# Kernel tuning notes

Hardware: AMD Instinct MI355X
Metric: run time of the kernel (lower is better)

## Reference

```python
import jax, jax.numpy as jnp
import numpy as np

D_MODEL = 2048
D_INNER = 4096
D_STATE = 16
DT_RANK = 128
D_CONV = 4
EPS = 1e-5


def setup_inputs() -> dict:
    key = jax.random.key(0)
    ks = jax.random.split(key, 10)
    b, l = 1, 1024
    s = 0.02
    x = jax.random.normal(ks[0], (b, l, D_MODEL), jnp.float32)
    w_norm = jnp.ones((D_MODEL,), jnp.float32)
    W_in = jax.random.normal(ks[1], (D_MODEL, 2 * D_INNER), jnp.float32) * s
    conv_w = jax.random.normal(ks[2], (D_CONV, D_INNER), jnp.float32) * 0.3
    conv_b = jnp.zeros((D_INNER,), jnp.float32)
    W_xp = jax.random.normal(ks[3], (D_INNER, DT_RANK + 2 * D_STATE), jnp.float32) * s
    W_dt = jax.random.normal(ks[4], (DT_RANK, D_INNER), jnp.float32) * s
    b_dt = jnp.full((D_INNER,), -4.0, jnp.float32)  # softplus(-4) ~ small dt
    A_log = jnp.log(jnp.tile(jnp.arange(1, D_STATE + 1, dtype=jnp.float32), (D_INNER, 1)))
    D = jnp.ones((D_INNER,), jnp.float32)
    W_out = jax.random.normal(ks[5], (D_INNER, D_MODEL), jnp.float32) * s
    return dict(x=x, w_norm=w_norm, W_in=W_in, conv_w=conv_w, conv_b=conv_b,
                W_xp=W_xp, W_dt=W_dt, b_dt=b_dt, A_log=A_log, D=D, W_out=W_out)


def _rmsnorm(x, w):
    return x * jax.lax.rsqrt(jnp.mean(jnp.square(x), axis=-1, keepdims=True) + EPS) * w


def _depthwise_causal_conv(x, conv_w, conv_b):
    # x: (b, l, d_inner), conv_w: (d_conv, d_inner)
    k = conv_w[:, None, :]  # (W, I/groups=1, O)
    y = jax.lax.conv_general_dilated(
        x, k, window_strides=(1,), padding=((D_CONV - 1, 0),),
        dimension_numbers=('NWC', 'WIO', 'NWC'), feature_group_count=D_INNER)
    return y + conv_b


def _selective_scan(u, delta, A, B, C, D):
    # u, delta: (b,l,d); A: (d,n); B,C: (b,l,n); D: (d,)
    deltaA = jnp.exp(jnp.einsum('bld,dn->bldn', delta, A))          # (b,l,d,n)
    deltaBu = jnp.einsum('bld,bln,bld->bldn', delta, B, u)          # (b,l,d,n)
    dA = jnp.moveaxis(deltaA, 1, 0)    # (l,b,d,n)
    dBu = jnp.moveaxis(deltaBu, 1, 0)  # (l,b,d,n)
    Ct = jnp.moveaxis(C, 1, 0)         # (l,b,n)
    b, l, d = u.shape
    n = A.shape[1]

    def step(h, inputs):
        dA_t, dBu_t, C_t = inputs
        h = h * dA_t + dBu_t                       # (b,d,n)
        y = jnp.einsum('bdn,bn->bd', h, C_t)       # (b,d)
        return h, y

    h0 = jnp.zeros((b, d, n), u.dtype)
    _, ys = jax.lax.scan(step, h0, (dA, dBu, Ct))
    y = jnp.moveaxis(ys, 0, 1)                     # (b,l,d)
    return y + u * D


def reference(x, w_norm, W_in, conv_w, conv_b, W_xp, W_dt, b_dt, A_log, D, W_out):
    # ResidualBlock: out = MambaBlock(RMSNorm(x)) + x
    xn = _rmsnorm(x, w_norm)
    xz = xn @ W_in                                  # (b,l,2*d_inner)
    xs, res = jnp.split(xz, 2, axis=-1)
    xs = _depthwise_causal_conv(xs, conv_w, conv_b)
    xs = jax.nn.silu(xs)
    # SSM
    A = -jnp.exp(A_log)                             # (d_inner, n)
    xdbc = xs @ W_xp                                # (b,l,dt_rank+2n)
    dt_r = xdbc[..., :DT_RANK]
    B = xdbc[..., DT_RANK:DT_RANK + D_STATE]
    C = xdbc[..., DT_RANK + D_STATE:]
    delta = jax.nn.softplus(dt_r @ W_dt + b_dt)     # (b,l,d_inner)
    y = _selective_scan(xs, delta, A, B, C, D)
    y = y * jax.nn.silu(res)
    out = y @ W_out + x
    return out
```

## Files before the change

kernel.cpp:

```cpp
#include <hip/hip_runtime.h>
#include <math.h>

#define L_SEQ   1024
#define DMODEL  2048
#define DINNER  4096
#define DSTATE  16
#define DTRANK  128
#define N_XZ    (2 * DINNER)
#define N_XP    (DTRANK + 2 * DSTATE)
#define EPS_F   1e-5f
#define NCHUNK  32
#define TCH     32
#define SK_XP   16

using bf16x8 = __attribute__((ext_vector_type(8))) short;
using f32x4  = __attribute__((ext_vector_type(4))) float;

__device__ __forceinline__ float silu_f(float v) {
    return v * (1.0f / (1.0f + __expf(-v)));
}
__device__ __forceinline__ float softplus_f(float v) {
    return (v > 15.0f) ? v : log1pf(__expf(v));
}
__device__ __forceinline__ unsigned short f2bf(float f) {
    unsigned b = __float_as_uint(f);
    return (unsigned short)((b + 0x7FFFu + ((b >> 16) & 1u)) >> 16);
}
__device__ __forceinline__ float bf2f(unsigned short u) {
    return __uint_as_float((unsigned)u << 16);
}

#define GLOAD_LDS(gp, lp) \
    __builtin_amdgcn_global_load_lds((const __attribute__((address_space(1))) void*)(gp), \
                                     (__attribute__((address_space(3))) void*)(lp), 16, 0, 0)

__device__ __forceinline__ void transpose_blocked(const float* __restrict__ W,
                                                  unsigned short* __restrict__ BTb,
                                                  int K, int N, int bx, int by,
                                                  unsigned short* Tb) {
    const int tid = threadIdx.x;
    const int n0 = bx * 64, k0 = by * 128;
    #pragma unroll
    for (int i = 0; i < 8; ++i) {
        const int r = i * 16 + (tid >> 4);
        const int c = (tid & 15) * 4;
        float4 v = *(const float4*)&W[(size_t)(k0 + r) * N + n0 + c];
        Tb[(c + 0) * 136 + r] = f2bf(v.x);
        Tb[(c + 1) * 136 + r] = f2bf(v.y);
        Tb[(c + 2) * 136 + r] = f2bf(v.z);
        Tb[(c + 3) * 136 + r] = f2bf(v.w);
    }
    __syncthreads();
    const int wave = tid >> 6, lane = tid & 63;
    const int kblocks = K >> 5;
    #pragma unroll
    for (int t = 0; t < 4; ++t) {
        const int ob = wave * 4 + t;
        const int nb = ob >> 2, kb = ob & 3;
        const int n = nb * 16 + (lane >> 2);
        const int k = kb * 32 + (lane & 3) * 8;
        bf16x8 v = *(const bf16x8*)&Tb[n * 136 + k];
        const size_t blk = (size_t)(((n0 >> 4) + nb)) * kblocks + ((k0 >> 5) + kb);
        *(bf16x8*)&BTb[blk * 512 + (size_t)lane * 8] = v;
    }
}

__device__ __forceinline__ void transpose_fast(const float* __restrict__ W,
                                               unsigned short* __restrict__ BT,
                                               int K, int N, int bx, int by) {
    const int wave = threadIdx.x >> 6, lane = threadIdx.x & 63;
    const int lr = lane >> 3, lc = lane & 7;
    const int k0 = by * 128 + (wave >> 1) * 64 + lr * 8;
    const int n0 = bx * 128 + (wave & 1) * 64 + lc * 8;
    float v[8][8];
    #pragma unroll
    for (int j = 0; j < 8; ++j) {
        float4 a = *(const float4*)&W[(size_t)(k0 + j) * N + n0];
        float4 b = *(const float4*)&W[(size_t)(k0 + j) * N + n0 + 4];
        v[j][0] = a.x; v[j][1] = a.y; v[j][2] = a.z; v[j][3] = a.w;
        v[j][4] = b.x; v[j][5] = b.y; v[j][6] = b.z; v[j][7] = b.w;
    }
    #pragma unroll
    for (int i = 0; i < 8; ++i) {
        bf16x8 o;
        #pragma unroll
        for (int j = 0; j < 8; ++j) o[j] = (short)f2bf(v[j][i]);
        *(bf16x8*)&BT[(size_t)(n0 + i) * K + k0] = o;
    }
}

__device__ __forceinline__ void transpose_body(const float* __restrict__ W,
                                               unsigned short* __restrict__ BT,
                                               int K, int N, int bx, int by,
                                               unsigned short (*Tl)[72]) {
    const int k0 = by * 64, n0 = bx * 32;
    const int kr = threadIdx.x >> 3;
    const int nc = (threadIdx.x & 7) * 4;
    float4 v0 = *(const float4*)&W[(size_t)(k0 + kr) * N + n0 + nc];
    float4 v1 = *(const float4*)&W[(size_t)(k0 + kr + 32) * N + n0 + nc];
    Tl[nc + 0][kr] = f2bf(v0.x); Tl[nc + 1][kr] = f2bf(v0.y);
    Tl[nc + 2][kr] = f2bf(v0.z); Tl[nc + 3][kr] = f2bf(v0.w);
    Tl[nc + 0][kr + 32] = f2bf(v1.x); Tl[nc + 1][kr + 32] = f2bf(v1.y);
    Tl[nc + 2][kr + 32] = f2bf(v1.z); Tl[nc + 3][kr + 32] = f2bf(v1.w);
    __syncthreads();
    const int n = threadIdx.x >> 3;
    const int k8 = (threadIdx.x & 7) * 8;
    *(bf16x8*)&BT[(size_t)(n0 + n) * K + k0 + k8] = *(const bf16x8*)&Tl[n][k8];
}

__global__ __launch_bounds__(256) void prep_win_kernel(const float* __restrict__ W_in,
                                                       unsigned short* __restrict__ BT_in) {
    __shared__ __align__(16) unsigned short Tb[64 * 136];
    transpose_blocked(W_in, BT_in, DMODEL, N_XZ, blockIdx.x & 127, blockIdx.x >> 7, Tb);
}

__global__ __launch_bounds__(256) void prep_rest_kernel(const float* __restrict__ W_xp,
                                                        const float* __restrict__ W_dt,
                                                        const float* __restrict__ W_out,
                                                        const float* __restrict__ x,
                                                        const float* __restrict__ wn,
                                                        unsigned short* __restrict__ BTxp,
                                                        unsigned short* __restrict__ BTdt,
                                                        unsigned short* __restrict__ BT_out,
                                                        unsigned short* __restrict__ xn_bf) {
    __shared__ __align__(16) unsigned short Tb[64 * 136];
    __shared__ unsigned short Tl[32][72];
    __shared__ float red[4];
    int b = blockIdx.x;
    if (b < 1024) {
        transpose_blocked(W_out, BT_out, DINNER, DMODEL, b & 31, b >> 5, Tb);
    } else if (b < 1056) {
        b -= 1024;
        transpose_fast(W_dt, BTdt, DTRANK, DINNER, b, 0);
    } else if (b < 1376) {
        b -= 1056;
        transpose_body(W_xp, BTxp, DINNER, N_XP, b % 5, b / 5, Tl);
    } else {
        const int row = b - 1376;
        const float4* xr = (const float4*)(x + (size_t)row * DMODEL);
        float ss = 0.f;
        float4 v0 = xr[threadIdx.x];
        float4 v1 = xr[threadIdx.x + 256];
        ss += v0.x*v0.x + v0.y*v0.y + v0.z*v0.z + v0.w*v0.w;
        ss += v1.x*v1.x + v1.y*v1.y + v1.z*v1.z + v1.w*v1.w;
        #pragma unroll
        for (int o = 32; o > 0; o >>= 1) ss += __shfl_down(ss, o);
        const int lane = threadIdx.x & 63, wv = threadIdx.x >> 6;
        if (lane == 0) red[wv] = ss;
        __syncthreads();
        if (threadIdx.x == 0) {
            float t = red[0] + red[1] + red[2] + red[3];
            red[0] = rsqrtf(t / (float)DMODEL + EPS_F);
        }
        __syncthreads();
        const float scale = red[0];
        const float4* wr = (const float4*)wn;
        float4 w0 = wr[threadIdx.x];
        float4 w1 = wr[threadIdx.x + 256];
        ushort4 o0, o1;
        o0.x = f2bf(v0.x * scale * w0.x); o0.y = f2bf(v0.y * scale * w0.y);
        o0.z = f2bf(v0.z * scale * w0.z); o0.w = f2bf(v0.w * scale * w0.w);
        o1.x = f2bf(v1.x * scale * w1.x); o1.y = f2bf(v1.y * scale * w1.y);
        o1.z = f2bf(v1.z * scale * w1.z); o1.w = f2bf(v1.w * scale * w1.w);
        unsigned short* outr = xn_bf + (size_t)row * DMODEL;
        *(ushort4*)&outr[threadIdx.x * 4] = o0;
        *(ushort4*)&outr[1024 + threadIdx.x * 4] = o1;
    }
}

template <int BM, int BN, int KC, int OUTM, int BLK>
__global__ __launch_bounds__(256) void gemm_mfma_kernel(const unsigned short* __restrict__ A,
                                                        const unsigned short* __restrict__ BT,
                                                        void* __restrict__ Cv,
                                                        int K, int Kc, int ldc, int Ncols,
                                                        const float* __restrict__ aux) {
    constexpr int MT = BM / 32;
    constexpr int NT = BN / 32;
    __shared__ __align__(16) unsigned short Al[KC * BM * 32];
    __shared__ __align__(16) unsigned short Bl[KC * BN * 32];
    const int tid = threadIdx.x;
    const int lane = tid & 63, wave = tid >> 6;
    const int wm = wave >> 1, wn = wave & 1;
    const int bm = blockIdx.y * BM, bn = blockIdx.x * BN;
    const size_t koff = (size_t)blockIdx.z * Kc;
    float* Cf = (float*)Cv;
    if (OUTM == 2) Cf += (size_t)blockIdx.z * (size_t)gridDim.y * BM * ldc;
    const int sr = lane >> 2;
    const int sk = (((lane & 3) ^ ((sr >> 1) & 3))) * 8;
    const int fr = lane & 15;
    const int fq = lane >> 4;
    const int fsw = (fq ^ ((fr >> 1) & 3)) * 8;

    f32x4 acc[MT][NT];
    #pragma unroll
    for (int i = 0; i < MT; ++i)
        #pragma unroll
        for (int j = 0; j < NT; ++j)
            acc[i][j] = (f32x4){0.f, 0.f, 0.f, 0.f};

    for (int k0 = 0; k0 < Kc; k0 += 32 * KC) {
        #pragma unroll
        for (int p = 0; p < KC; ++p) {
            #pragma unroll
            for (int is = wave; is < BM / 16; is += 4)
                GLOAD_LDS(&A[(size_t)(bm + is * 16 + sr) * K + koff + k0 + p * 32 + sk],
                          &Al[p * BM * 32 + is * 512]);
            #pragma unroll
            for (int is = wave; is < BN / 16; is += 4) {
                if (BLK) {
                    const size_t blk = (size_t)((bn >> 4) + is) * (K >> 5)
                                     + ((koff + k0 + p * 32) >> 5);
                    GLOAD_LDS(&BT[blk * 512 + sr * 32 + sk],
                              &Bl[p * BN * 32 + is * 512]);
                } else {
                    GLOAD_LDS(&BT[(size_t)(bn + is * 16 + sr) * K + koff + k0 + p * 32 + sk],
                              &Bl[p * BN * 32 + is * 512]);
                }
            }
        }
        __syncthreads();
        #pragma unroll
        for (int p = 0; p < KC; ++p) {
            bf16x8 af[MT], bfr[NT];
            #pragma unroll
            for (int i = 0; i < MT; ++i)
                af[i] = *(const bf16x8*)&Al[p * BM * 32 + (wm * (BM / 2) + i * 16 + fr) * 32 + fsw];
            #pragma unroll
            for (int j = 0; j < NT; ++j)
                bfr[j] = *(const bf16x8*)&Bl[p * BN * 32 + (wn * (BN / 2) + j * 16 + fr) * 32 + fsw];
            #pragma unroll
            for (int i = 0; i < MT; ++i)
                #pragma unroll
                for (int j = 0; j < NT; ++j)
                    acc[i][j] = __builtin_amdgcn_mfma_f32_16x16x32_bf16(af[i], bfr[j], acc[i][j], 0, 0, 0);
        }
        __syncthreads();
    }

    #pragma unroll
    for (int i = 0; i < MT; ++i) {
        const int row = bm + wm * (BM / 2) + i * 16 + fq * 4;
        #pragma unroll
        for (int j = 0; j < NT; ++j) {
            const int col = bn + wn * (BN / 2) + j * 16 + fr;
            if (col < Ncols) {
                #pragma unroll
                for (int r = 0; r < 4; ++r) {
                    float v = acc[i][j][r];
                    if (OUTM == 0) {
                        ((unsigned short*)Cv)[(size_t)(row + r) * ldc + col] = f2bf(v);
                    } else {
                        Cf[(size_t)(row + r) * ldc + col] = v;
                    }
                }
            }
        }
    }
}

__global__ __launch_bounds__(256) void gemm_k128_softplus_kernel(
        const unsigned short* __restrict__ A,
        const unsigned short* __restrict__ BT,
        unsigned short* __restrict__ C,
        const float* __restrict__ bias) {
    const int lane = threadIdx.x & 63, wave = threadIdx.x >> 6;
    const int wm = wave >> 1, wn = wave & 1;
    const int fr = lane & 15, fq = lane >> 4;
    const int bm = blockIdx.y * 64, bn = blockIdx.x * 64;

    bf16x8 af[2][4], bfr[2][4];
    #pragma unroll
    for (int i = 0; i < 2; ++i) {
        const unsigned short* Ap = &A[(size_t)(bm + wm * 32 + i * 16 + fr) * DTRANK + fq * 8];
        #pragma unroll
        for (int kc = 0; kc < 4; ++kc) af[i][kc] = *(const bf16x8*)&Ap[kc * 32];
    }
    #pragma unroll
    for (int j = 0; j < 2; ++j) {
        const unsigned short* Bp = &BT[(size_t)(bn + wn * 32 + j * 16 + fr) * DTRANK + fq * 8];
        #pragma unroll
        for (int kc = 0; kc < 4; ++kc) bfr[j][kc] = *(const bf16x8*)&Bp[kc * 32];
    }

    f32x4 acc[2][2];
    #pragma unroll
    for (int i = 0; i < 2; ++i)
        #pragma unroll
        for (int j = 0; j < 2; ++j)
            acc[i][j] = (f32x4){0.f, 0.f, 0.f, 0.f};
    #pragma unroll
    for (int kc = 0; kc < 4; ++kc)
        #pragma unroll
        for (int i = 0; i < 2; ++i)
            #pragma unroll
            for (int j = 0; j < 2; ++j)
                acc[i][j] = __builtin_amdgcn_mfma_f32_16x16x32_bf16(af[i][kc], bfr[j][kc], acc[i][j], 0, 0, 0);

    #pragma unroll
    for (int i = 0; i < 2; ++i) {
        const int row = bm + wm * 32 + i * 16 + fq * 4;
        #pragma unroll
        for (int j = 0; j < 2; ++j) {
            const int col = bn + wn * 32 + j * 16 + fr;
            const float bc = bias[col];
            #pragma unroll
            for (int r = 0; r < 4; ++r)
                C[(size_t)(row + r) * DINNER + col] = f2bf(softplus_f(acc[i][j][r] + bc));
        }
    }
}

__global__ __launch_bounds__(256) void conv_silu_kernel(const unsigned short* __restrict__ xz_bf,
                                                        const float* __restrict__ cw,
                                                        const float* __restrict__ cb,
                                                        unsigned short* __restrict__ xs_bf) {
    const int idx = blockIdx.x * 256 + threadIdx.x;
    const int t = idx >> 9;
    const int c8 = (idx & 511) * 8;
    float acc[8];
    {
        float4 b0 = *(const float4*)&cb[c8];
        float4 b1 = *(const float4*)&cb[c8 + 4];
        acc[0] = b0.x; acc[1] = b0.y; acc[2] = b0.z; acc[3] = b0.w;
        acc[4] = b1.x; acc[5] = b1.y; acc[6] = b1.z; acc[7] = b1.w;
    }
    #pragma unroll
    for (int k = 0; k < 4; ++k) {
        const int tt = t + k - 3;
        if (tt >= 0) {
            bf16x8 xv = *(const bf16x8*)&xz_bf[(size_t)tt * N_XZ + c8];
            float4 w0 = *(const float4*)&cw[k * DINNER + c8];
            float4 w1 = *(const float4*)&cw[k * DINNER + c8 + 4];
            acc[0] = fmaf(bf2f((unsigned short)xv[0]), w0.x, acc[0]);
            acc[1] = fmaf(bf2f((unsigned short)xv[1]), w0.y, acc[1]);
            acc[2] = fmaf(bf2f((unsigned short)xv[2]), w0.z, acc[2]);
            acc[3] = fmaf(bf2f((unsigned short)xv[3]), w0.w, acc[3]);
            acc[4] = fmaf(bf2f((unsigned short)xv[4]), w1.x, acc[4]);
            acc[5] = fmaf(bf2f((unsigned short)xv[5]), w1.y, acc[5]);
            acc[6] = fmaf(bf2f((unsigned short)xv[6]), w1.z, acc[6]);
            acc[7] = fmaf(bf2f((unsigned short)xv[7]), w1.w, acc[7]);
        }
    }
    bf16x8 o;
    #pragma unroll
    for (int q = 0; q < 8; ++q) o[q] = (short)f2bf(silu_f(acc[q]));
    *(bf16x8*)&xs_bf[(size_t)t * DINNER + c8] = o;
}

__global__ __launch_bounds__(256) void reduce_sk_kernel(const float* __restrict__ part,
                                                        float* __restrict__ xdbc,
                                                        unsigned short* __restrict__ xdbc_dt) {
    const int i = (blockIdx.x * 256 + threadIdx.x) * 4;
    float4 s = make_float4(0.f, 0.f, 0.f, 0.f);
    #pragma unroll
    for (int c = 0; c < SK_XP; ++c) {
        float4 v = *(const float4*)&part[(size_t)c * (L_SEQ * N_XP) + i];
        s.x += v.x; s.y += v.y; s.z += v.z; s.w += v.w;
    }
    *(float4*)&xdbc[i] = s;
    const int col = i % N_XP;
    if (col < DTRANK) {
        ushort4 o;
        o.x = f2bf(s.x); o.y = f2bf(s.y); o.z = f2bf(s.z); o.w = f2bf(s.w);
        *(ushort4*)&xdbc_dt[(i / N_XP) * DTRANK + col] = o;
    }
}

__global__ __launch_bounds__(256) void reduce2_res_kernel(const float* __restrict__ part,
                                                          const float* __restrict__ x,
                                                          float* __restrict__ out) {
    const size_t i = ((size_t)blockIdx.x * 256 + threadIdx.x) * 4;
    float4 a = *(const float4*)&part[i];
    float4 b = *(const float4*)&part[(size_t)L_SEQ * DMODEL + i];
    float4 r = *(const float4*)&x[i];
    float4 o;
    o.x = a.x + b.x + r.x;
    o.y = a.y + b.y + r.y;
    o.z = a.z + b.z + r.z;
    o.w = a.w + b.w + r.w;
    *(float4*)&out[i] = o;
}

__global__ __launch_bounds__(256) void scan_pass1(const unsigned short* __restrict__ delta_bf,
                                                  const unsigned short* __restrict__ xs_bf,
                                                  const float* __restrict__ xdbc,
                                                  const float* __restrict__ A_log,
                                                  float* __restrict__ S,
                                                  float* __restrict__ sumdl) {
    __shared__ float BC[TCH][32];
    __shared__ __align__(16) unsigned short DL[TCH][256];
    __shared__ __align__(16) unsigned short US[TCH][256];
    const int c = blockIdx.y;
    const int tid = threadIdx.x;
    const int d0 = blockIdx.x * 256;
    const int d = d0 + tid;
    const int t0 = c * TCH;
    {
        const int tt = tid >> 3, q = tid & 7;
        *(float4*)&BC[tt][q * 4] =
            *(const float4*)&xdbc[(size_t)(t0 + tt) * N_XP + DTRANK + q * 4];
    }
    #pragma unroll
    for (int u = 0; u < 4; ++u) {
        const int l = tid + 256 * u;
        const int r = l >> 5, cc = (l & 31) * 8;
        *(bf16x8*)&DL[r][cc] = *(const bf16x8*)&delta_bf[(size_t)(t0 + r) * DINNER + d0 + cc];
        *(bf16x8*)&US[r][cc] = *(const bf16x8*)&xs_bf[(size_t)(t0 + r) * DINNER + d0 + cc];
    }
    __syncthreads();
    float Aa[16];
    #pragma unroll
    for (int n = 0; n < 16; n += 4) {
        float4 a = *(const float4*)&A_log[(size_t)d * 16 + n];
        Aa[n]     = -__expf(a.x); Aa[n + 1] = -__expf(a.y);
        Aa[n + 2] = -__expf(a.z); Aa[n + 3] = -__expf(a.w);
    }
    float h[16];
    #pragma unroll
    for (int n = 0; n < 16; ++n) h[n] = 0.f;
    float sd = 0.f;
    for (int t = 0; t < TCH; ++t) {
        const float dl = bf2f(DL[t][tid]);
        const float u  = bf2f(US[t][tid]);
        sd += dl;
        const float du = dl * u;
        #pragma unroll
        for (int n = 0; n < 16; ++n)
            h[n] = fmaf(h[n], __expf(dl * Aa[n]), du * BC[t][n]);
    }
    float* Sp = &S[((size_t)c * DINNER + d) * 16];
    #pragma unroll
    for (int n = 0; n < 16; n += 4)
        *(float4*)&Sp[n] = make_float4(h[n], h[n + 1], h[n + 2], h[n + 3]);
    sumdl[c * DINNER + d] = sd;
}

__global__ __launch_bounds__(256) void scan_pass2(const float* __restrict__ S,
                                                  const float* __restrict__ sumdl,
                                                  const float* __restrict__ A_log,
                                                  float* __restrict__ h0) {
    const int i = blockIdx.x * 256 + threadIdx.x;
    const int dd = i >> 4;
    const float A = -__expf(A_log[i]);
    float h = 0.f;
    #pragma unroll
    for (int c = 0; c < NCHUNK; ++c) {
        h0[(size_t)c * (DINNER * 16) + i] = h;
        h = h * __expf(A * sumdl[c * DINNER + dd]) + S[(size_t)c * (DINNER * 16) + i];
    }
}

__global__ __launch_bounds__(256) void scan_pass3(const unsigned short* __restrict__ delta_bf,
                                                  const unsigned short* __restrict__ xs_bf,
                                                  const float* __restrict__ xdbc,
                                                  const unsigned short* __restrict__ xz_bf,
                                                  const float* __restrict__ A_log,
                                                  const float* __restrict__ Dp,
                                                  const float* __restrict__ h0,
                                                  unsigned short* __restrict__ yg_bf) {
    __shared__ float BC[TCH][32];
    __shared__ __align__(16) unsigned short DL[TCH][256];
    __shared__ __align__(16) unsigned short US[TCH][256];
    __shared__ __align__(16) unsigned short RS[TCH][256];
    __shared__ __align__(16) unsigned short YG[TCH][256];
    const int c = blockIdx.y;
    const int tid = threadIdx.x;
    const int d0 = blockIdx.x * 256;
    const int d = d0 + tid;
    const int t0 = c * TCH;
    {
        const int tt = tid >> 3, q = tid & 7;
        *(float4*)&BC[tt][q * 4] =
            *(const float4*)&xdbc[(size_t)(t0 + tt) * N_XP + DTRANK + q * 4];
    }
    #pragma unroll
    for (int u = 0; u < 4; ++u) {
        const int l = tid + 256 * u;
        const int r = l >> 5, cc = (l & 31) * 8;
        *(bf16x8*)&DL[r][cc] = *(const bf16x8*)&delta_bf[(size_t)(t0 + r) * DINNER + d0 + cc];
        *(bf16x8*)&US[r][cc] = *(const bf16x8*)&xs_bf[(size_t)(t0 + r) * DINNER + d0 + cc];
        *(bf16x8*)&RS[r][cc] =
            *(const bf16x8*)&xz_bf[(size_t)(t0 + r) * N_XZ + DINNER + d0 + cc];
    }
    __syncthreads();
    float Aa[16];
    #pragma unroll
    for (int n = 0; n < 16; n += 4) {
        float4 a = *(const float4*)&A_log[(size_t)d * 16 + n];
        Aa[n]     = -__expf(a.x); Aa[n + 1] = -__expf(a.y);
        Aa[n + 2] = -__expf(a.z); Aa[n + 3] = -__expf(a.w);
    }
    float h[16];
    const float* h0p = &h0[(size_t)c * (DINNER * 16) + d * 16];
    #pragma unroll
    for (int n = 0; n < 16; n += 4) {
        float4 v = *(const float4*)&h0p[n];
        h[n] = v.x; h[n + 1] = v.y; h[n + 2] = v.z; h[n + 3] = v.w;
    }
    const float Dd = Dp[d];
    for (int t = 0; t < TCH; ++t) {
        const float dl = bf2f(DL[t][tid]);
        const float u  = bf2f(US[t][tid]);
        const float du = dl * u;
        float y = 0.f;
        #pragma unroll
        for (int n = 0; n < 16; ++n) {
            h[n] = fmaf(h[n], __expf(dl * Aa[n]), du * BC[t][n]);
            y = fmaf(h[n], BC[t][16 + n], y);
        }
        const float res = bf2f(RS[t][tid]);
        YG[t][tid] = f2bf((y + u * Dd) * silu_f(res));
    }
    __syncthreads();
    #pragma unroll
    for (int u = 0; u < 4; ++u) {
        const int l = tid + 256 * u;
        const int r = l >> 5, cc = (l & 31) * 8;
        *(bf16x8*)&yg_bf[(size_t)(t0 + r) * DINNER + d0 + cc] = *(const bf16x8*)&YG[r][cc];
    }
}

extern "C" void kernel_launch(void* const* d_in, const int* in_sizes, int n_in,
                              void* d_out, int out_size, void* d_ws, size_t ws_size,
                              hipStream_t stream) {
    const float* x     = (const float*)d_in[0];
    const float* wn    = (const float*)d_in[1];
    const float* W_in  = (const float*)d_in[2];
    const float* cw    = (const float*)d_in[3];
    const float* cb    = (const float*)d_in[4];
    const float* W_xp  = (const float*)d_in[5];
    const float* W_dt  = (const float*)d_in[6];
    const float* b_dt  = (const float*)d_in[7];
    const float* A_log = (const float*)d_in[8];
    const float* Dp    = (const float*)d_in[9];
    const float* W_out = (const float*)d_in[10];
    float* out = (float*)d_out;

    float* ws = (float*)d_ws;
    unsigned short* xz_bf    = (unsigned short*)ws;
    unsigned short* xs_bf    = (unsigned short*)(ws + 4194304);
    unsigned short* yg_bf    = (unsigned short*)(ws + 6291456);
    unsigned short* delta_bf = (unsigned short*)(ws + 8388608);
    float*          part     = ws + 10485760;
    float*          S        = ws + 13107200;
    float*          sumdl    = ws + 15204352;
    float*          h0       = ws + 15335424;
    float*          xdbc     = ws + 17432576;
    unsigned short* xn_bf    = (unsigned short*)(ws + 17596416);
    unsigned short* BTxp     = (unsigned short*)(ws + 18644992);
    unsigned short* BTdt     = (unsigned short*)(ws + 18972672);
    unsigned short* xdbc_dt  = (unsigned short*)(ws + 19234816);
    unsigned short* BT_in    = (unsigned short*)(ws + 19300352);
    unsigned short* BT_out   = (unsigned short*)(ws + 27688960);

    prep_win_kernel<<<2048, 256, 0, stream>>>(W_in, BT_in);
    prep_rest_kernel<<<2400, 256, 0, stream>>>(W_xp, W_dt, W_out, x, wn,
                                               BTxp, BTdt, BT_out, xn_bf);
    gemm_mfma_kernel<128, 128, 2, 0, 1><<<dim3(N_XZ / 128, L_SEQ / 128), 256, 0, stream>>>(
        xn_bf, BT_in, xz_bf, DMODEL, DMODEL, N_XZ, N_XZ, nullptr);
    conv_silu_kernel<<<(L_SEQ * DINNER / 8) / 256, 256, 0, stream>>>(xz_bf, cw, cb, xs_bf);
    gemm_mfma_kernel<64, 64, 2, 2, 0><<<dim3(3, L_SEQ / 64, SK_XP), 256, 0, stream>>>(
        xs_bf, BTxp, part, DINNER, DINNER / SK_XP, N_XP, N_XP, nullptr);
    reduce_sk_kernel<<<(L_SEQ * N_XP / 4) / 256, 256, 0, stream>>>(part, xdbc, xdbc_dt);
    gemm_k128_softplus_kernel<<<dim3(DINNER / 64, L_SEQ / 64), 256, 0, stream>>>(
        xdbc_dt, BTdt, delta_bf, b_dt);
    scan_pass1<<<dim3(DINNER / 256, NCHUNK), 256, 0, stream>>>(delta_bf, xs_bf, xdbc, A_log, S, sumdl);
    scan_pass2<<<(DINNER * 16) / 256, 256, 0, stream>>>(S, sumdl, A_log, h0);
    scan_pass3<<<dim3(DINNER / 256, NCHUNK), 256, 0, stream>>>(delta_bf, xs_bf, xdbc, xz_bf,
                                                               A_log, Dp, h0, yg_bf);
    gemm_mfma_kernel<64, 128, 2, 2, 1><<<dim3(DMODEL / 128, L_SEQ / 64, 2), 256, 0, stream>>>(
        yg_bf, BT_out, part, DINNER, DINNER / 2, DMODEL, DMODEL, nullptr);
    reduce2_res_kernel<<<(L_SEQ * DMODEL) / 1024, 256, 0, stream>>>(part, x, out);
}
```

Baseline: 323.3 us.

## Fuse delta projection GEMM into scan pass1 and merge prep kernels

Computes the dt_rank→d_inner projection with softplus inside scan_pass1. Each block runs MFMA on its 32-timestep by 256-channel tile and writes delta straight into shared memory. It still writes delta to global memory for pass3. This removes one kernel launch and the global re-read of delta in pass1. The two weight-prep kernels are also merged into one launch. The cost is more register pressure and MFMA work at the head of the scan kernel.

```diff
diff --git a/kernel.cpp b/kernel.cpp
--- a/kernel.cpp
+++ b/kernel.cpp
@@ -108,35 +108,34 @@
     *(bf16x8*)&BT[(size_t)(n0 + n) * K + k0 + k8] = *(const bf16x8*)&Tl[n][k8];
 }
 
-__global__ __launch_bounds__(256) void prep_win_kernel(const float* __restrict__ W_in,
-                                                       unsigned short* __restrict__ BT_in) {
-    __shared__ __align__(16) unsigned short Tb[64 * 136];
-    transpose_blocked(W_in, BT_in, DMODEL, N_XZ, blockIdx.x & 127, blockIdx.x >> 7, Tb);
-}
-
-__global__ __launch_bounds__(256) void prep_rest_kernel(const float* __restrict__ W_xp,
-                                                        const float* __restrict__ W_dt,
-                                                        const float* __restrict__ W_out,
-                                                        const float* __restrict__ x,
-                                                        const float* __restrict__ wn,
-                                                        unsigned short* __restrict__ BTxp,
-                                                        unsigned short* __restrict__ BTdt,
-                                                        unsigned short* __restrict__ BT_out,
-                                                        unsigned short* __restrict__ xn_bf) {
+__global__ __launch_bounds__(256) void prep_kernel(const float* __restrict__ W_in,
+                                                   const float* __restrict__ W_xp,
+                                                   const float* __restrict__ W_dt,
+                                                   const float* __restrict__ W_out,
+                                                   const float* __restrict__ x,
+                                                   const float* __restrict__ wn,
+                                                   unsigned short* __restrict__ BT_in,
+                                                   unsigned short* __restrict__ BTxp,
+                                                   unsigned short* __restrict__ BTdt,
+                                                   unsigned short* __restrict__ BT_out,
+                                                   unsigned short* __restrict__ xn_bf) {
     __shared__ __align__(16) unsigned short Tb[64 * 136];
     __shared__ unsigned short Tl[32][72];
     __shared__ float red[4];
     int b = blockIdx.x;
-    if (b < 1024) {
+    if (b < 2048) {
+        transpose_blocked(W_in, BT_in, DMODEL, N_XZ, b & 127, b >> 7, Tb);
+    } else if (b < 3072) {
+        b -= 2048;
         transpose_blocked(W_out, BT_out, DINNER, DMODEL, b & 31, b >> 5, Tb);
-    } else if (b < 1056) {
-        b -= 1024;
+    } else if (b < 3104) {
+        b -= 3072;
         transpose_fast(W_dt, BTdt, DTRANK, DINNER, b, 0);
-    } else if (b < 1376) {
-        b -= 1056;
+    } else if (b < 3424) {
+        b -= 3104;
         transpose_body(W_xp, BTxp, DINNER, N_XP, b % 5, b / 5, Tl);
     } else {
-        const int row = b - 1376;
+        const int row = b - 3424;
         const float4* xr = (const float4*)(x + (size_t)row * DMODEL);
         float ss = 0.f;
         float4 v0 = xr[threadIdx.x];
@@ -258,58 +257,6 @@
     }
 }
 
-__global__ __launch_bounds__(256) void gemm_k128_softplus_kernel(
-        const unsigned short* __restrict__ A,
-        const unsigned short* __restrict__ BT,
-        unsigned short* __restrict__ C,
-        const float* __restrict__ bias) {
-    const int lane = threadIdx.x & 63, wave = threadIdx.x >> 6;
-    const int wm = wave >> 1, wn = wave & 1;
-    const int fr = lane & 15, fq = lane >> 4;
-    const int bm = blockIdx.y * 64, bn = blockIdx.x * 64;
-
-    bf16x8 af[2][4], bfr[2][4];
-    #pragma unroll
-    for (int i = 0; i < 2; ++i) {
-        const unsigned short* Ap = &A[(size_t)(bm + wm * 32 + i * 16 + fr) * DTRANK + fq * 8];
-        #pragma unroll
-        for (int kc = 0; kc < 4; ++kc) af[i][kc] = *(const bf16x8*)&Ap[kc * 32];
-    }
-    #pragma unroll
-    for (int j = 0; j < 2; ++j) {
-        const unsigned short* Bp = &BT[(size_t)(bn + wn * 32 + j * 16 + fr) * DTRANK + fq * 8];
-        #pragma unroll
-        for (int kc = 0; kc < 4; ++kc) bfr[j][kc] = *(const bf16x8*)&Bp[kc * 32];
-    }
-
-    f32x4 acc[2][2];
-    #pragma unroll
-    for (int i = 0; i < 2; ++i)
-        #pragma unroll
-        for (int j = 0; j < 2; ++j)
-            acc[i][j] = (f32x4){0.f, 0.f, 0.f, 0.f};
-    #pragma unroll
-    for (int kc = 0; kc < 4; ++kc)
-        #pragma unroll
-        for (int i = 0; i < 2; ++i)
-            #pragma unroll
-            for (int j = 0; j < 2; ++j)
-                acc[i][j] = __builtin_amdgcn_mfma_f32_16x16x32_bf16(af[i][kc], bfr[j][kc], acc[i][j], 0, 0, 0);
-
-    #pragma unroll
-    for (int i = 0; i < 2; ++i) {
-        const int row = bm + wm * 32 + i * 16 + fq * 4;
-        #pragma unroll
-        for (int j = 0; j < 2; ++j) {
-            const int col = bn + wn * 32 + j * 16 + fr;
-            const float bc = bias[col];
-            #pragma unroll
-            for (int r = 0; r < 4; ++r)
-                C[(size_t)(row + r) * DINNER + col] = f2bf(softplus_f(acc[i][j][r] + bc));
-        }
-    }
-}
-
 __global__ __launch_bounds__(256) void conv_silu_kernel(const unsigned short* __restrict__ xz_bf,
                                                         const float* __restrict__ cw,
                                                         const float* __restrict__ cb,
@@ -381,10 +328,13 @@
     *(float4*)&out[i] = o;
 }
 
-__global__ __launch_bounds__(256) void scan_pass1(const unsigned short* __restrict__ delta_bf,
+__global__ __launch_bounds__(256) void scan_pass1(const unsigned short* __restrict__ xdbc_dt,
+                                                  const unsigned short* __restrict__ BTdt,
+                                                  const float* __restrict__ b_dt,
                                                   const unsigned short* __restrict__ xs_bf,
                                                   const float* __restrict__ xdbc,
                                                   const float* __restrict__ A_log,
+                                                  unsigned short* __restrict__ delta_bf,
                                                   float* __restrict__ S,
                                                   float* __restrict__ sumdl) {
     __shared__ float BC[TCH][32];
@@ -395,6 +345,51 @@
     const int d0 = blockIdx.x * 256;
     const int d = d0 + tid;
     const int t0 = c * TCH;
+    const int lane = tid & 63, wave = tid >> 6;
+    const int fr = lane & 15, fq = lane >> 4;
+
+    bf16x8 af[2][4], bfr[4][4];
+    #pragma unroll
+    for (int i = 0; i < 2; ++i) {
+        const unsigned short* Ap = &xdbc_dt[(size_t)(t0 + i * 16 + fr) * DTRANK + fq * 8];
+        #pragma unroll
+        for (int kc = 0; kc < 4; ++kc) af[i][kc] = *(const bf16x8*)&Ap[kc * 32];
+    }
+    #pragma unroll
+    for (int j = 0; j < 4; ++j) {
+        const unsigned short* Bp = &BTdt[(size_t)(d0 + wave * 64 + j * 16 + fr) * DTRANK + fq * 8];
+        #pragma unroll
+        for (int kc = 0; kc < 4; ++kc) bfr[j][kc] = *(const bf16x8*)&Bp[kc * 32];
+    }
+    f32x4 acc[2][4];
+    #pragma unroll
+    for (int i = 0; i < 2; ++i)
+        #pragma unroll
+        for (int j = 0; j < 4; ++j)
+            acc[i][j] = (f32x4){0.f, 0.f, 0.f, 0.f};
+    #pragma unroll
+    for (int kc = 0; kc < 4; ++kc)
+        #pragma unroll
+        for (int i = 0; i < 2; ++i)
+            #pragma unroll
+            for (int j = 0; j < 4; ++j)
+                acc[i][j] = __builtin_amdgcn_mfma_f32_16x16x32_bf16(af[i][kc], bfr[j][kc], acc[i][j], 0, 0, 0);
+    #pragma unroll
+    for (int i = 0; i < 2; ++i) {
+        #pragma unroll
+        for (int j = 0; j < 4; ++j) {
+            const int col = wave * 64 + j * 16 + fr;
+            const float bc = b_dt[d0 + col];
+            #pragma unroll
+            for (int r = 0; r < 4; ++r) {
+                const int row = i * 16 + fq * 4 + r;
+                const unsigned short dv = f2bf(softplus_f(acc[i][j][r] + bc));
+                DL[row][col] = dv;
+                delta_bf[(size_t)(t0 + row) * DINNER + d0 + col] = dv;
+            }
+        }
+    }
+
     {
         const int tt = tid >> 3, q = tid & 7;
         *(float4*)&BC[tt][q * 4] =
@@ -404,10 +399,10 @@
     for (int u = 0; u < 4; ++u) {
         const int l = tid + 256 * u;
         const int r = l >> 5, cc = (l & 31) * 8;
-        *(bf16x8*)&DL[r][cc] = *(const bf16x8*)&delta_bf[(size_t)(t0 + r) * DINNER + d0 + cc];
         *(bf16x8*)&US[r][cc] = *(const bf16x8*)&xs_bf[(size_t)(t0 + r) * DINNER + d0 + cc];
     }
     __syncthreads();
+
     float Aa[16];
     #pragma unroll
     for (int n = 0; n < 16; n += 4) {
@@ -553,18 +548,16 @@
     unsigned short* BT_in    = (unsigned short*)(ws + 19300352);
     unsigned short* BT_out   = (unsigned short*)(ws + 27688960);
 
-    prep_win_kernel<<<2048, 256, 0, stream>>>(W_in, BT_in);
-    prep_rest_kernel<<<2400, 256, 0, stream>>>(W_xp, W_dt, W_out, x, wn,
-                                               BTxp, BTdt, BT_out, xn_bf);
+    prep_kernel<<<4448, 256, 0, stream>>>(W_in, W_xp, W_dt, W_out, x, wn,
+                                          BT_in, BTxp, BTdt, BT_out, xn_bf);
     gemm_mfma_kernel<128, 128, 2, 0, 1><<<dim3(N_XZ / 128, L_SEQ / 128), 256, 0, stream>>>(
         xn_bf, BT_in, xz_bf, DMODEL, DMODEL, N_XZ, N_XZ, nullptr);
     conv_silu_kernel<<<(L_SEQ * DINNER / 8) / 256, 256, 0, stream>>>(xz_bf, cw, cb, xs_bf);
     gemm_mfma_kernel<64, 64, 2, 2, 0><<<dim3(3, L_SEQ / 64, SK_XP), 256, 0, stream>>>(
         xs_bf, BTxp, part, DINNER, DINNER / SK_XP, N_XP, N_XP, nullptr);
     reduce_sk_kernel<<<(L_SEQ * N_XP / 4) / 256, 256, 0, stream>>>(part, xdbc, xdbc_dt);
-    gemm_k128_softplus_kernel<<<dim3(DINNER / 64, L_SEQ / 64), 256, 0, stream>>>(
-        xdbc_dt, BTdt, delta_bf, b_dt);
-    scan_pass1<<<dim3(DINNER / 256, NCHUNK), 256, 0, stream>>>(delta_bf, xs_bf, xdbc, A_log, S, sumdl);
+    scan_pass1<<<dim3(DINNER / 256, NCHUNK), 256, 0, stream>>>(
+        xdbc_dt, BTdt, b_dt, xs_bf, xdbc, A_log, delta_bf, S, sumdl);
     scan_pass2<<<(DINNER * 16) / 256, 256, 0, stream>>>(S, sumdl, A_log, h0);
     scan_pass3<<<dim3(DINNER / 256, NCHUNK), 256, 0, stream>>>(delta_bf, xs_bf, xdbc, xz_bf,
                                                                A_log, Dp, h0, yg_bf);
```

After: 318.3 us. About the same (-1.5%).
